# Kernel tuning notes

Measured on AMD Instinct MI355X. Metric: run time of the kernel, lower is better.

The kernel has to match this reference:

```python
import jax, jax.numpy as jnp
import numpy as np

B, S = 32, 128          # batch, seq_len
C, K = 256, 128         # num_concept, dim_k (== dim_e == dim_correct)
DC = 128                # dim_correct
NQ, NIT, NUT = 10000, 1024, 1024


def _xavier(k, shape):
    fan_out, fan_in = shape[0], shape[1]
    bound = float(np.sqrt(6.0 / (fan_in + fan_out)))
    return jax.random.uniform(k, shape, jnp.float32, -bound, bound)


def setup_inputs() -> dict:
    key = jax.random.key(0)
    ks = jax.random.split(key, 16)
    question_seq = jax.random.randint(ks[0], (B, S), 0, NQ + 1)
    interval_time_seq = jax.random.randint(ks[1], (B, S), 0, NIT + 1)
    use_time_seq = jax.random.randint(ks[2], (B, S), 0, NUT + 1)
    correct_seq = jnp.round(jax.random.uniform(ks[3], (B, S))).astype(jnp.float32)
    E_q = _xavier(ks[4], (NQ + 1, K))
    E_it = _xavier(ks[5], (NIT + 1, K))
    E_ut = _xavier(ks[6], (NUT + 1, K))
    q_matrix = (jax.random.uniform(ks[7], (NQ + 1, C)) < 0.03).astype(jnp.float32)
    h0 = _xavier(ks[8], (C, K))  # xavier init of the initial concept memory
    W1 = _xavier(ks[9], (K, K + K + DC)); b1 = jnp.zeros((K,), jnp.float32)
    W2 = _xavier(ks[10], (K, 4 * K));     b2 = jnp.zeros((K,), jnp.float32)
    W3 = _xavier(ks[11], (K, 4 * K));     b3 = jnp.zeros((K,), jnp.float32)
    W4 = _xavier(ks[12], (K, 3 * K));     b4 = jnp.zeros((K,), jnp.float32)
    W5 = _xavier(ks[13], (K, 2 * K));     b5 = jnp.zeros((K,), jnp.float32)
    return dict(question_seq=question_seq, interval_time_seq=interval_time_seq,
                use_time_seq=use_time_seq, correct_seq=correct_seq,
                E_q=E_q, E_it=E_it, E_ut=E_ut, q_matrix=q_matrix, h0=h0,
                W1=W1, b1=b1, W2=W2, b2=b2, W3=W3, b3=b3,
                W4=W4, b4=b4, W5=W5, b5=b5)


def _forward(question_seq, interval_time_seq, use_time_seq, correct_seq,
             E_q, E_it, E_ut, q_matrix, h0,
             W1, b1, W2, b2, W3, b3, W4, b4, W5, b5):
    bsz, slen = question_seq.shape
    dim_k = h0.shape[1]
    dim_c = W1.shape[1] - 2 * dim_k

    q_emb = E_q[question_seq]            # [B,S,K]
    it_emb = E_it[interval_time_seq]     # [B,S,K]
    ut_emb = E_ut[use_time_seq]          # [B,S,K]
    c_emb = jnp.broadcast_to(correct_seq[..., None], (bsz, slen, dim_c))
    all_learning = jnp.concatenate([q_emb, ut_emb, c_emb], -1) @ W1.T + b1  # [B,S,K]
    qe = q_matrix[question_seq]          # [B,S,C]

    h_pre0 = jnp.tile(h0[None], (bsz, 1, 1))                     # [B,C,K]
    h_tilde0 = jnp.einsum('bc,bck->bk', qe[:, 0], h_pre0)        # q_e @ h at t=0
    learning0 = jnp.zeros((bsz, dim_k), all_learning.dtype)

    # split linear_4 weight over its (h_pre, LG, it) concat blocks
    W4h, W4l, W4i = W4[:, :dim_k], W4[:, dim_k:2 * dim_k], W4[:, 2 * dim_k:]

    # time-major per-step inputs for t = 0 .. S-2
    xs = (jnp.swapaxes(it_emb[:, :-1], 0, 1),
          jnp.swapaxes(all_learning[:, :-1], 0, 1),
          jnp.swapaxes(qe[:, :-1], 0, 1),
          jnp.swapaxes(qe[:, 1:], 0, 1),
          jnp.swapaxes(q_emb[:, 1:], 0, 1))

    def step(carry, x):
        h_pre, h_tilde_pre, learning_pre = carry
        it, learning, qe_t, qe_n, qemb_n = x
        cat = jnp.concatenate([learning_pre, it, learning, h_tilde_pre], -1)  # [B,4K]
        learning_gain = jnp.tanh(cat @ W2.T + b2)
        gamma_l = jax.nn.sigmoid(cat @ W3.T + b3)
        LG = gamma_l * (learning_gain + 1.0) * 0.5                 # [B,K]
        LG_tilde = qe_t[:, :, None] * LG[:, None, :]               # [B,C,K] outer write
        gamma_f = jax.nn.sigmoid(jnp.einsum('bck,jk->bcj', h_pre, W4h)
                                 + (LG @ W4l.T + it @ W4i.T + b4)[:, None, :])
        h = LG_tilde + gamma_f * h_pre                             # [B,C,K]
        h_tilde = jnp.einsum('bc,bck->bk', qe_n, h)                # read for t+1
        y = jax.nn.sigmoid(jnp.concatenate([qemb_n, h_tilde], -1) @ W5.T + b5).sum(-1) / dim_k
        return (h, h_tilde, learning), y

    _, ys = jax.lax.scan(step, (h_pre0, h_tilde0, learning0), xs)  # ys: [S-1,B]
    pred = jnp.concatenate([jnp.zeros((bsz, 1), ys.dtype), ys.T], axis=1)
    return pred


def reference(question_seq, interval_time_seq, use_time_seq, correct_seq,
              E_q, E_it, E_ut, q_matrix, h0,
              W1, b1, W2, b2, W3, b3, W4, b4, W5, b5):
    return _forward(question_seq, interval_time_seq, use_time_seq, correct_seq,
                    E_q, E_it, E_ut, q_matrix, h0,
                    W1, b1, W2, b2, W3, b3, W4, b4, W5, b5)
```

## Files before the change

kernel.cpp:

```cpp
#include <hip/hip_runtime.h>
#include <hip/hip_bf16.h>


typedef __bf16 bf16x8 __attribute__((ext_vector_type(8)));
typedef __bf16 bf16x4 __attribute__((ext_vector_type(4)));
typedef float f32x4 __attribute__((ext_vector_type(4)));

#define HBUF 32768

__device__ __forceinline__ float sigmf(float x){
  return __builtin_amdgcn_rcpf(1.0f + __expf(-x));
}

__device__ __forceinline__ bf16x8 cvt8(float4 a, float4 b){
  bf16x8 r;
  r[0]=(__bf16)a.x; r[1]=(__bf16)a.y; r[2]=(__bf16)a.z; r[3]=(__bf16)a.w;
  r[4]=(__bf16)b.x; r[5]=(__bf16)b.y; r[6]=(__bf16)b.z; r[7]=(__bf16)b.w;
  return r;
}

__device__ __forceinline__ void mk_hilo(float4 a, float4 b, bf16x8& hi, bf16x8& lo){
  float v[8] = {a.x,a.y,a.z,a.w,b.x,b.y,b.z,b.w};
  #pragma unroll
  for (int i = 0; i < 8; i++){
    __bf16 h = (__bf16)v[i];
    hi[i] = h;
    lo[i] = (__bf16)(v[i] - (float)h);
  }
}

__device__ __forceinline__ f32x4 mfma16(bf16x8 a, bf16x8 b, f32x4 c){
  return __builtin_amdgcn_mfma_f32_16x16x32_bf16(a, b, c, 0, 0, 0);
}

__device__ __forceinline__ float dpp_sum16(float v){
  int x;
  x = __builtin_amdgcn_update_dpp(0, __builtin_bit_cast(int, v), 0x111, 0xf, 0xf, true);
  v += __builtin_bit_cast(float, x);
  x = __builtin_amdgcn_update_dpp(0, __builtin_bit_cast(int, v), 0x112, 0xf, 0xf, true);
  v += __builtin_bit_cast(float, x);
  x = __builtin_amdgcn_update_dpp(0, __builtin_bit_cast(int, v), 0x114, 0xf, 0xf, true);
  v += __builtin_bit_cast(float, x);
  x = __builtin_amdgcn_update_dpp(0, __builtin_bit_cast(int, v), 0x118, 0xf, 0xf, true);
  v += __builtin_bit_cast(float, x);
  return v;
}

__device__ __forceinline__ void red16(f32x4& r){
  r[0] = dpp_sum16(r[0]);
  r[1] = dpp_sum16(r[1]);
  r[2] = dpp_sum16(r[2]);
  r[3] = dpp_sum16(r[3]);
}

__global__ __launch_bounds__(256) void k1_al(
    const int* __restrict__ qseq, const int* __restrict__ utseq,
    const float* __restrict__ corr,
    const float* __restrict__ Eq, const float* __restrict__ Eut,
    const float* __restrict__ W1, const float* __restrict__ b1,
    const float* __restrict__ W5, const float* __restrict__ b5,
    float* __restrict__ AL, float* __restrict__ pre5)
{
  __shared__ __bf16 inA[64*256];
  __shared__ float corrs[64];
  __shared__ float b1s[128], b5s[128], rsp[256];
  const int tid = threadIdx.x, blk = blockIdx.x;
  if (tid < 128){ b1s[tid]=b1[tid]; b5s[tid]=b5[tid]; }
  {
    int j = tid & 127, hf = tid >> 7;
    const float* p = W1 + j*384 + 256 + hf*64;
    float s = 0.f;
    for (int i = 0; i < 64; i++) s += p[i];
    rsp[tid] = s;
  }
  {
    int r = tid >> 2, seg = tid & 3;
    int R = blk*64 + r;
    int qi = qseq[R], ui = utseq[R];
    if (seg == 0) corrs[r] = corr[R];
    for (int i = 0; i < 64; i++){
      int col = seg*64 + i;
      float v = (col < 128) ? Eq[qi*128 + col] : Eut[ui*128 + (col-128)];
      inA[((r*256 + col) ^ ((r&7)<<3))] = (__bf16)v;
    }
  }
  __syncthreads();
  const int w = tid >> 6, lane = tid & 63;
  const int la = lane & 15, g = lane >> 4;
  const int rbase = w*16;
  bf16x8 af[8];
  #pragma unroll
  for (int kt = 0; kt < 8; kt++){
    int idx = ((rbase+la)*256 + kt*32 + g*8) ^ ((la&7)<<3);
    af[kt] = *(const bf16x8*)&inA[idx];
  }
  for (int jt = 0; jt < 8; jt++){
    f32x4 acc = {0.f,0.f,0.f,0.f};
    const float* Wb = W1 + (jt*16+la)*384;
    #pragma unroll
    for (int kt = 0; kt < 8; kt++){
      const float* p = Wb + kt*32 + g*8;
      acc = mfma16(af[kt], cvt8(*(const float4*)p, *(const float4*)(p+4)), acc);
    }
    int j = jt*16 + la;
    float rsj = rsp[j] + rsp[j+128];
    #pragma unroll
    for (int rr = 0; rr < 4; rr++){
      int row = rbase + g*4 + rr;
      int R = blk*64 + row;
      AL[R*128 + j] = acc[rr] + b1s[j] + corrs[row]*rsj;
    }
  }
  for (int jt = 0; jt < 8; jt++){
    f32x4 acc = {0.f,0.f,0.f,0.f};
    const float* Wb = W5 + (jt*16+la)*256;
    #pragma unroll
    for (int kt = 0; kt < 4; kt++){
      const float* p = Wb + kt*32 + g*8;
      acc = mfma16(af[kt], cvt8(*(const float4*)p, *(const float4*)(p+4)), acc);
    }
    int j = jt*16 + la;
    #pragma unroll
    for (int rr = 0; rr < 4; rr++){
      int row = rbase + g*4 + rr;
      int R = blk*64 + row;
      pre5[R*128 + j] = acc[rr] + b5s[j];
    }
  }
}

__global__ __launch_bounds__(256) void k2_pre(
    const int* __restrict__ itseq, const float* __restrict__ Eit,
    const float* __restrict__ AL,
    const float* __restrict__ W2, const float* __restrict__ W3,
    const float* __restrict__ W4,
    const float* __restrict__ b2, const float* __restrict__ b3,
    const float* __restrict__ b4,
    float* __restrict__ pre23, float* __restrict__ pre4)
{
  __shared__ __bf16 inA[64*384];
  __shared__ int obase[64];
  __shared__ float b2s[128], b3s[128], b4s[128];
  const int tid = threadIdx.x, blk = blockIdx.x;
  if (tid < 128){ b2s[tid]=b2[tid]; b3s[tid]=b3[tid]; b4s[tid]=b4[tid]; }
  {
    int r = tid >> 2, seg = tid & 3;
    int R = blk*64 + r;
    bool valid = (R < 4064);
    int b_ = R / 127, tau = R % 127;
    if (seg == 0) obase[r] = valid ? (b_*127 + tau) : -1;
    int itv = valid ? itseq[b_*128 + tau] : 0;
    for (int i = 0; i < 96; i++){
      int col = seg*96 + i;
      float v = 0.f;
      if (valid){
        if (col < 128)      v = (tau > 0) ? AL[(b_*128 + tau-1)*128 + col] : 0.f;
        else if (col < 256) v = Eit[itv*128 + (col-128)];
        else                v = AL[(b_*128 + tau)*128 + (col-256)];
      }
      inA[((r*384 + col) ^ ((r&7)<<3))] = (__bf16)v;
    }
  }
  __syncthreads();
  const int w = tid >> 6, lane = tid & 63;
  const int la = lane & 15, g = lane >> 4;
  const int rbase = w*16;
  bf16x8 af[12];
  #pragma unroll
  for (int kt = 0; kt < 12; kt++){
    int idx = ((rbase+la)*384 + kt*32 + g*8) ^ ((la&7)<<3);
    af[kt] = *(const bf16x8*)&inA[idx];
  }
  for (int jt = 0; jt < 16; jt++){
    f32x4 acc = {0.f,0.f,0.f,0.f};
    int j = jt*16 + la;
    const float* Wb = (j < 128) ? (W2 + j*512) : (W3 + (j-128)*512);
    #pragma unroll
    for (int kt = 0; kt < 12; kt++){
      const float* p = Wb + kt*32 + g*8;
      acc = mfma16(af[kt], cvt8(*(const float4*)p, *(const float4*)(p+4)), acc);
    }
    float bias = (j < 128) ? b2s[j] : b3s[j-128];
    #pragma unroll
    for (int rr = 0; rr < 4; rr++){
      int row = rbase + g*4 + rr;
      int ob = obase[row];
      if (ob >= 0) pre23[ob*256 + j] = acc[rr] + bias;
    }
  }
  for (int jt = 0; jt < 8; jt++){
    f32x4 acc = {0.f,0.f,0.f,0.f};
    int j = jt*16 + la;
    const float* Wb = W4 + j*384 + 256;
    #pragma unroll
    for (int kk = 0; kk < 4; kk++){
      const float* p = Wb + kk*32 + g*8;
      acc = mfma16(af[4+kk], cvt8(*(const float4*)p, *(const float4*)(p+4)), acc);
    }
    #pragma unroll
    for (int rr = 0; rr < 4; rr++){
      int row = rbase + g*4 + rr;
      int ob = obase[row];
      if (ob >= 0) pre4[ob*128 + j] = acc[rr] + b4s[j];
    }
  }
}

#define SCAN_LDS_BYTES (35136*4)

__global__ __launch_bounds__(512, 2) void lpkt_scan(
    const float* __restrict__ qmat, const int* __restrict__ qseq,
    const float* __restrict__ h0,
    const float* __restrict__ W2, const float* __restrict__ W3,
    const float* __restrict__ W4,
    const float* __restrict__ pre23, const float* __restrict__ pre4,
    float* __restrict__ hist)
{
  extern __shared__ float lds[];
  __bf16* hB   = (__bf16*)lds;
  float*  htb0 = lds + 32768;
  float*  htb1 = lds + 33024;
  float*  LGb  = lds + 33280;
  __bf16* LGh  = (__bf16*)(lds + 33408);
  float*  qeb  = lds + 33472;
  float*  p23L = lds + 34240;
  float*  p4L  = lds + 34752;
  int*    qsl  = (int*)(lds + 35008);

  const int tid  = threadIdx.x;
  const int b    = blockIdx.x;
  const int lane = tid & 63;
  const int w    = tid >> 6;
  const int la   = lane & 15, g = lane >> 4;
  const int jq   = w & 3;
  const int ch   = w >> 2;

  bf16x8 af[2][4];
  bf16x8 af4l[2][4];
  #pragma unroll
  for (int jj = 0; jj < 2; jj++){
    #pragma unroll
    for (int kt = 0; kt < 4; kt++){
      const float* ph = W4 + ((jq*2+jj)*16+la)*384 + kt*32 + g*8;
      const float* pl = W4 + ((jq*2+jj)*16+la)*384 + 128 + kt*32 + g*8;
      af[jj][kt]   = cvt8(*(const float4*)ph, *(const float4*)(ph+4));
      af4l[jj][kt] = cvt8(*(const float4*)pl, *(const float4*)(pl+4));
    }
  }
  bf16x8 af23[2][4];
  #pragma unroll
  for (int kt = 0; kt < 4; kt++){
    const float* p2 = W2 + (w*16+la)*512 + 384 + kt*32 + g*8;
    const float* p3 = W3 + (w*16+la)*512 + 384 + kt*32 + g*8;
    af23[0][kt] = cvt8(*(const float4*)p2, *(const float4*)(p2+4));
    af23[1][kt] = cvt8(*(const float4*)p3, *(const float4*)(p3+4));
  }

  int rb[8], wb[8];
  #pragma unroll
  for (int cg = 0; cg < 8; cg++){
    const int cblk = ch*8 + cg;
    rb[cg] = cblk*2048 + g*128 + la*8;
    wb[cg] = cblk*2048 + jq*512 + (g>>1)*128 + la*8 + (g&1)*4;
  }

  if (tid < 128) qsl[tid] = qseq[b*128 + tid];
  __syncthreads();
  const float* pre23b = pre23 + b*127*256;
  const float* pre4b  = pre4  + b*127*128;
  if (tid < 64)       *(float4*)&qeb[tid*4] = *(const float4*)(qmat + (size_t)qsl[0]*256 + tid*4);
  else if (tid < 128) *(float4*)&qeb[256 + (tid-64)*4] = *(const float4*)(qmat + (size_t)qsl[1]*256 + (tid-64)*4);
  else if (tid < 192) *(float4*)&p23L[(tid-128)*4] = *(const float4*)(pre23b + (tid-128)*4);
  else if (tid < 224) *(float4*)&p4L[(tid-192)*4]  = *(const float4*)(pre4b  + (tid-192)*4);

  float4 hreg[8][2];
  #pragma unroll
  for (int cg = 0; cg < 8; cg++){
    const int c_ = ch*128 + cg*16 + la;
    #pragma unroll
    for (int jj = 0; jj < 2; jj++){
      const int k0 = (jq*2+jj)*16 + g*4;
      float4 v = *(const float4*)(h0 + c_*128 + k0);
      hreg[cg][jj] = v;
      bf16x4 hb; hb[0]=(__bf16)v.x; hb[1]=(__bf16)v.y; hb[2]=(__bf16)v.z; hb[3]=(__bf16)v.w;
      *(bf16x4*)&hB[wb[cg] + jj*256] = hb;
    }
  }
  __syncthreads();
  {
    f32x4 r0 = {0.f,0.f,0.f,0.f}, r1 = {0.f,0.f,0.f,0.f};
    #pragma unroll
    for (int cg = 0; cg < 8; cg++){
      const int c_ = ch*128 + cg*16 + la;
      float q = qeb[c_];
      float4 h0v = hreg[cg][0], h1v = hreg[cg][1];
      r0[0] += q*h0v.x; r0[1] += q*h0v.y; r0[2] += q*h0v.z; r0[3] += q*h0v.w;
      r1[0] += q*h1v.x; r1[1] += q*h1v.y; r1[2] += q*h1v.z; r1[3] += q*h1v.w;
    }
    red16(r0); red16(r1);
    if (la == 15){
      float4 s0 = {r0[0],r0[1],r0[2],r0[3]};
      float4 s1 = {r1[0],r1[1],r1[2],r1[3]};
      *(float4*)&htb0[ch*128 + jq*32 + g*4]      = s0;
      *(float4*)&htb0[ch*128 + jq*32 + 16 + g*4] = s1;
    }
  }
  __syncthreads();

  int i0 = 0, i1 = 1, i2 = 2;

  for (int tau = 0; tau < 127; tau++){
    float* htc = (tau & 1) ? htb1 : htb0;
    float* htn = (tau & 1) ? htb0 : htb1;
    float* qec = qeb + i0*256;
    float* qen = qeb + i1*256;
    float* qep = qeb + i2*256;
    const float* p23c = p23L + (tau & 1)*256;
    const float* p4c  = p4L  + (tau & 1)*128;
    const int roff = (tau & 1) ? HBUF : 0;
    const int woff = (tau & 1) ? 0 : HBUF;

    {
      bf16x8 xh[4], xl[4];
      #pragma unroll
      for (int kt = 0; kt < 4; kt++){
        int k0 = kt*32 + g*8;
        float4 a0 = *(const float4*)&htc[k0];
        float4 a1 = *(const float4*)&htc[k0+4];
        float4 b0 = *(const float4*)&htc[128 + k0];
        float4 b1v = *(const float4*)&htc[128 + k0+4];
        a0.x += b0.x; a0.y += b0.y; a0.z += b0.z; a0.w += b0.w;
        a1.x += b1v.x; a1.y += b1v.y; a1.z += b1v.z; a1.w += b1v.w;
        mk_hilo(a0, a1, xh[kt], xl[kt]);
      }
      f32x4 aLh = {0.f,0.f,0.f,0.f}, aLl = {0.f,0.f,0.f,0.f};
      f32x4 aGh = {0.f,0.f,0.f,0.f}, aGl = {0.f,0.f,0.f,0.f};
      #pragma unroll
      for (int kt = 0; kt < 4; kt++){
        aLh = mfma16(af23[0][kt], xh[kt], aLh);
        aLl = mfma16(af23[0][kt], xl[kt], aLl);
        aGh = mfma16(af23[1][kt], xh[kt], aGh);
        aGl = mfma16(af23[1][kt], xl[kt], aGl);
      }
      float4 lp4 = *(const float4*)&p23c[w*16 + g*4];
      float4 gp4 = *(const float4*)&p23c[128 + w*16 + g*4];
      float4 LG4;
      LG4.x = sigmf(aGh[0]+aGl[0]+gp4.x) * sigmf(2.f*(aLh[0]+aLl[0]+lp4.x));
      LG4.y = sigmf(aGh[1]+aGl[1]+gp4.y) * sigmf(2.f*(aLh[1]+aLl[1]+lp4.y));
      LG4.z = sigmf(aGh[2]+aGl[2]+gp4.z) * sigmf(2.f*(aLh[2]+aLl[2]+lp4.z));
      LG4.w = sigmf(aGh[3]+aGl[3]+gp4.w) * sigmf(2.f*(aLh[3]+aLl[3]+lp4.w));
      if (la == 0){
        *(float4*)&LGb[w*16 + g*4] = LG4;
        bf16x4 lgp;
        lgp[0]=(__bf16)LG4.x; lgp[1]=(__bf16)LG4.y;
        lgp[2]=(__bf16)LG4.z; lgp[3]=(__bf16)LG4.w;
        *(bf16x4*)&LGh[w*16 + g*4] = lgp;
      }
    }
    __syncthreads();

    float4 pf23, pf4, pfqe;
    const bool dopf = (tau < 126);
    const bool do23 = dopf && (tid < 64);
    const bool do4  = dopf && (tid >= 64) && (tid < 96);
    const bool doqe = dopf && (tid >= 448);
    if (do23) pf23 = *(const float4*)(pre23b + (tau+1)*256 + tid*4);
    if (do4)  pf4  = *(const float4*)(pre4b  + (tau+1)*128 + (tid-64)*4);
    if (doqe) pfqe = *(const float4*)(qmat + (size_t)qsl[tau+2]*256 + (tid-448)*4);
    if (tau > 0 && tid >= 96 && tid < 128){
      int i = (tid - 96)*4;
      float4 v0 = *(const float4*)&htc[i];
      float4 v1 = *(const float4*)&htc[128 + i];
      float4 v = {v0.x+v1.x, v0.y+v1.y, v0.z+v1.z, v0.w+v1.w};
      *(float4*)(hist + ((size_t)b*127 + (tau-1))*128 + i) = v;
    }

    float4 z4[2];
    {
      bf16x8 lh[4];
      #pragma unroll
      for (int kt = 0; kt < 4; kt++)
        lh[kt] = *(const bf16x8*)&LGh[kt*32 + g*8];
      #pragma unroll
      for (int jj = 0; jj < 2; jj++){
        f32x4 az = {0.f,0.f,0.f,0.f};
        #pragma unroll
        for (int kt = 0; kt < 4; kt++)
          az = mfma16(af4l[jj][kt], lh[kt], az);
        float4 zp = *(const float4*)&p4c[(jq*2+jj)*16 + g*4];
        z4[jj].x = az[0]+zp.x; z4[jj].y = az[1]+zp.y;
        z4[jj].z = az[2]+zp.z; z4[jj].w = az[3]+zp.w;
      }
    }
    float4 lg4[2];
    #pragma unroll
    for (int jj = 0; jj < 2; jj++)
      lg4[jj] = *(const float4*)&LGb[(jq*2+jj)*16 + g*4];

    bf16x8 bA[4], bB[4];
    {
      const int base = rb[0] + roff;
      #pragma unroll
      for (int kt = 0; kt < 4; kt++) bA[kt] = *(const bf16x8*)&hB[base + kt*512];
    }
    f32x4 r0 = {0.f,0.f,0.f,0.f}, r1 = {0.f,0.f,0.f,0.f};
    #pragma unroll
    for (int cg = 0; cg < 8; cg++){
      const bf16x8* cur = (cg & 1) ? bB : bA;
      bf16x8*       nxt = (cg & 1) ? bA : bB;
      if (cg < 7){
        const int base = rb[cg+1] + roff;
        #pragma unroll
        for (int kt = 0; kt < 4; kt++) nxt[kt] = *(const bf16x8*)&hB[base + kt*512];
      }
      const int c_ = ch*128 + cg*16 + la;
      const float qe_t = qec[c_], qe_n = qen[c_];
      const int wbase = wb[cg] + woff;
      #pragma unroll
      for (int jj = 0; jj < 2; jj++){
        f32x4 acc = {0.f,0.f,0.f,0.f};
        #pragma unroll
        for (int kt = 0; kt < 4; kt++)
          acc = mfma16(af[jj][kt], cur[kt], acc);
        float4 hp = hreg[cg][jj];
        float4 hn;
        hn.x = qe_t*lg4[jj].x + sigmf(acc[0] + z4[jj].x)*hp.x;
        hn.y = qe_t*lg4[jj].y + sigmf(acc[1] + z4[jj].y)*hp.y;
        hn.z = qe_t*lg4[jj].z + sigmf(acc[2] + z4[jj].z)*hp.z;
        hn.w = qe_t*lg4[jj].w + sigmf(acc[3] + z4[jj].w)*hp.w;
        hreg[cg][jj] = hn;
        bf16x4 hb; hb[0]=(__bf16)hn.x; hb[1]=(__bf16)hn.y; hb[2]=(__bf16)hn.z; hb[3]=(__bf16)hn.w;
        *(bf16x4*)&hB[wbase + jj*256] = hb;
        f32x4& r = (jj == 0) ? r0 : r1;
        r[0] += qe_n*hn.x; r[1] += qe_n*hn.y;
        r[2] += qe_n*hn.z; r[3] += qe_n*hn.w;
      }
    }
    red16(r0); red16(r1);
    if (la == 15){
      float4 s0 = {r0[0],r0[1],r0[2],r0[3]};
      float4 s1 = {r1[0],r1[1],r1[2],r1[3]};
      *(float4*)&htn[ch*128 + jq*32 + g*4]      = s0;
      *(float4*)&htn[ch*128 + jq*32 + 16 + g*4] = s1;
    }
    if (do23) *(float4*)&p23L[((tau+1)&1)*256 + tid*4] = pf23;
    if (do4)  *(float4*)&p4L[((tau+1)&1)*128 + (tid-64)*4] = pf4;
    if (doqe) *(float4*)&qep[(tid-448)*4] = pfqe;
    __syncthreads();
    int t_ = i0; i0 = i1; i1 = i2; i2 = t_;
  }

  if (tid < 32){
    int i = tid*4;
    float4 v0 = *(const float4*)&htb1[i];
    float4 v1 = *(const float4*)&htb1[128 + i];
    float4 v = {v0.x+v1.x, v0.y+v1.y, v0.z+v1.z, v0.w+v1.w};
    *(float4*)(hist + ((size_t)b*127 + 126)*128 + i) = v;
  }
}

__global__ __launch_bounds__(128) void k4_y(
    const float* __restrict__ hist, const float* __restrict__ pre5,
    const float* __restrict__ W5, float* __restrict__ out)
{
  const int R = blockIdx.x;
  const int s = R & 127, b = R >> 7;
  const int j = threadIdx.x;
  __shared__ float xs[128];
  __shared__ float partial[2];
  if (s == 0){ if (j == 0) out[R] = 0.f; return; }
  xs[j] = hist[((size_t)b*127 + (s-1))*128 + j];
  __syncthreads();
  const float* wr = W5 + j*256 + 128;
  float acc = pre5[(size_t)R*128 + j];
  #pragma unroll
  for (int k = 0; k < 128; k += 4){
    float4 wv = *(const float4*)&wr[k];
    float4 xv = *(const float4*)&xs[k];
    acc += wv.x*xv.x + wv.y*xv.y + wv.z*xv.z + wv.w*xv.w;
  }
  float v = sigmf(acc);
  #pragma unroll
  for (int m = 1; m < 64; m <<= 1) v += __shfl_xor(v, m);
  if ((j & 63) == 0) partial[j >> 6] = v;
  __syncthreads();
  if (j == 0) out[R] = (partial[0] + partial[1]) * (1.f/128.f);
}

extern "C" void kernel_launch(void* const* d_in, const int* in_sizes, int n_in,
                              void* d_out, int out_size, void* d_ws, size_t ws_size,
                              hipStream_t stream) {
  const int*   qseq  = (const int*)  d_in[0];
  const int*   itseq = (const int*)  d_in[1];
  const int*   utseq = (const int*)  d_in[2];
  const float* corr  = (const float*)d_in[3];
  const float* Eq    = (const float*)d_in[4];
  const float* Eit   = (const float*)d_in[5];
  const float* Eut   = (const float*)d_in[6];
  const float* qmat  = (const float*)d_in[7];
  const float* h0    = (const float*)d_in[8];
  const float* W1    = (const float*)d_in[9];
  const float* b1    = (const float*)d_in[10];
  const float* W2    = (const float*)d_in[11];
  const float* b2    = (const float*)d_in[12];
  const float* W3    = (const float*)d_in[13];
  const float* b3    = (const float*)d_in[14];
  const float* W4    = (const float*)d_in[15];
  const float* b4    = (const float*)d_in[16];
  const float* W5    = (const float*)d_in[17];
  const float* b5    = (const float*)d_in[18];
  float* out = (float*)d_out;

  float* ws    = (float*)d_ws;
  float* AL    = ws;
  float* hist  = ws;
  float* pre5  = ws + 524288;
  float* pre23 = ws + 1048576;
  float* pre4  = ws + 2088960;

  (void)hipFuncSetAttribute(reinterpret_cast<const void*>(&lpkt_scan),
                            hipFuncAttributeMaxDynamicSharedMemorySize,
                            SCAN_LDS_BYTES);

  hipLaunchKernelGGL(k1_al, dim3(64), dim3(256), 0, stream,
                     qseq, utseq, corr, Eq, Eut, W1, b1, W5, b5, AL, pre5);
  hipLaunchKernelGGL(k2_pre, dim3(64), dim3(256), 0, stream,
                     itseq, Eit, AL, W2, W3, W4, b2, b3, b4, pre23, pre4);
  hipLaunchKernelGGL(lpkt_scan, dim3(32), dim3(512), SCAN_LDS_BYTES, stream,
                     qmat, qseq, h0, W2, W3, W4, pre23, pre4, hist);
  hipLaunchKernelGGL(k4_y, dim3(4096), dim3(128), 0, stream,
                     hist, pre5, W5, out);
}
```

Measured before the change: 821.8 us.

## Split each batch's concept memory across two workgroups with global-memory flag exchange

The recurrent scan now launches two workgroups per batch element, each owning half of the 256 concepts and half the LDS state. Every step, each half publishes its partial h_tilde read to a global buffer and sets a release flag, then spin-waits on the peer's flag before summing both partials. This doubles the number of CUs working on the latency-bound serial scan and halves per-block work per step. In exchange it adds a cross-workgroup handshake per timestep through global memory, assumes both peer blocks are co-resident, and carries a bounded spin that could silently continue with stale data.

```diff
diff --git a/kernel.cpp b/kernel.cpp
--- a/kernel.cpp
+++ b/kernel.cpp
@@ -6,7 +6,7 @@
 typedef __bf16 bf16x4 __attribute__((ext_vector_type(4)));
 typedef float f32x4 __attribute__((ext_vector_type(4)));
 
-#define HBUF 32768
+#define HBUF 16384
 
 __device__ __forceinline__ float sigmf(float x){
   return __builtin_amdgcn_rcpf(1.0f + __expf(-x));
@@ -206,7 +206,7 @@
   }
 }
 
-#define SCAN_LDS_BYTES (35136*4)
+#define SCAN_LDS_BYTES (18752*4)
 
 __global__ __launch_bounds__(512, 2) void lpkt_scan(
     const float* __restrict__ qmat, const int* __restrict__ qseq,
@@ -214,27 +214,34 @@
     const float* __restrict__ W2, const float* __restrict__ W3,
     const float* __restrict__ W4,
     const float* __restrict__ pre23, const float* __restrict__ pre4,
-    float* __restrict__ hist)
+    float* __restrict__ hist, float* __restrict__ xbuf, int* __restrict__ flags)
 {
   extern __shared__ float lds[];
   __bf16* hB   = (__bf16*)lds;
-  float*  htb0 = lds + 32768;
-  float*  htb1 = lds + 33024;
-  float*  LGb  = lds + 33280;
-  __bf16* LGh  = (__bf16*)(lds + 33408);
-  float*  qeb  = lds + 33472;
-  float*  p23L = lds + 34240;
-  float*  p4L  = lds + 34752;
-  int*    qsl  = (int*)(lds + 35008);
+  float*  htb0 = lds + 16384;
+  float*  htb1 = lds + 16640;
+  float*  LGb  = lds + 16896;
+  __bf16* LGh  = (__bf16*)(lds + 17024);
+  float*  qeb  = lds + 17088;
+  float*  p23L = lds + 17856;
+  float*  p4L  = lds + 18368;
+  int*    qsl  = (int*)(lds + 18624);
 
   const int tid  = threadIdx.x;
-  const int b    = blockIdx.x;
+  const int bid  = blockIdx.x;
+  const int half = bid >> 5;
+  const int b    = bid & 31;
   const int lane = tid & 63;
   const int w    = tid >> 6;
   const int la   = lane & 15, g = lane >> 4;
   const int jq   = w & 3;
   const int ch   = w >> 2;
 
+  float* xmine = xbuf + ((size_t)(b*2 + half))*128*128;
+  const float* xpeer = xbuf + ((size_t)(b*2 + (half^1)))*128*128;
+  int* fmine = flags + (b*2 + half)*128;
+  const int* fpeer = flags + (b*2 + (half^1))*128;
+
   bf16x8 af[2][4];
   bf16x8 af4l[2][4];
   #pragma unroll
@@ -256,10 +263,10 @@
     af23[1][kt] = cvt8(*(const float4*)p3, *(const float4*)(p3+4));
   }
 
-  int rb[8], wb[8];
-  #pragma unroll
-  for (int cg = 0; cg < 8; cg++){
-    const int cblk = ch*8 + cg;
+  int rb[4], wb[4];
+  #pragma unroll
+  for (int cg = 0; cg < 4; cg++){
+    const int cblk = ch*4 + cg;
     rb[cg] = cblk*2048 + g*128 + la*8;
     wb[cg] = cblk*2048 + jq*512 + (g>>1)*128 + la*8 + (g&1)*4;
   }
@@ -273,10 +280,10 @@
   else if (tid < 192) *(float4*)&p23L[(tid-128)*4] = *(const float4*)(pre23b + (tid-128)*4);
   else if (tid < 224) *(float4*)&p4L[(tid-192)*4]  = *(const float4*)(pre4b  + (tid-192)*4);
 
-  float4 hreg[8][2];
-  #pragma unroll
-  for (int cg = 0; cg < 8; cg++){
-    const int c_ = ch*128 + cg*16 + la;
+  float4 hreg[4][2];
+  #pragma unroll
+  for (int cg = 0; cg < 4; cg++){
+    const int c_ = half*128 + ch*64 + cg*16 + la;
     #pragma unroll
     for (int jj = 0; jj < 2; jj++){
       const int k0 = (jq*2+jj)*16 + g*4;
@@ -290,8 +297,8 @@
   {
     f32x4 r0 = {0.f,0.f,0.f,0.f}, r1 = {0.f,0.f,0.f,0.f};
     #pragma unroll
-    for (int cg = 0; cg < 8; cg++){
-      const int c_ = ch*128 + cg*16 + la;
+    for (int cg = 0; cg < 4; cg++){
+      const int c_ = half*128 + ch*64 + cg*16 + la;
       float q = qeb[c_];
       float4 h0v = hreg[cg][0], h1v = hreg[cg][1];
       r0[0] += q*h0v.x; r0[1] += q*h0v.y; r0[2] += q*h0v.z; r0[3] += q*h0v.w;
@@ -320,6 +327,26 @@
     const int roff = (tau & 1) ? HBUF : 0;
     const int woff = (tau & 1) ? 0 : HBUF;
 
+    if (w == 0){
+      if (lane < 32){
+        float4 v0 = *(const float4*)&htc[lane*4];
+        float4 v1 = *(const float4*)&htc[128 + lane*4];
+        float4 v = {v0.x+v1.x, v0.y+v1.y, v0.z+v1.z, v0.w+v1.w};
+        *(float4*)(xmine + (size_t)tau*128 + lane*4) = v;
+      }
+      __threadfence();
+      if (lane == 0)
+        __hip_atomic_store(&fmine[tau], 1, __ATOMIC_RELEASE, __HIP_MEMORY_SCOPE_AGENT);
+    }
+    {
+      int it = 0;
+      while (__hip_atomic_load(&fpeer[tau], __ATOMIC_ACQUIRE, __HIP_MEMORY_SCOPE_AGENT) == 0){
+        __builtin_amdgcn_s_sleep(2);
+        if (++it > (1 << 22)) break;
+      }
+    }
+    const float* xp = xpeer + (size_t)tau*128;
+
     {
       bf16x8 xh[4], xl[4];
       #pragma unroll
@@ -329,8 +356,12 @@
         float4 a1 = *(const float4*)&htc[k0+4];
         float4 b0 = *(const float4*)&htc[128 + k0];
         float4 b1v = *(const float4*)&htc[128 + k0+4];
-        a0.x += b0.x; a0.y += b0.y; a0.z += b0.z; a0.w += b0.w;
-        a1.x += b1v.x; a1.y += b1v.y; a1.z += b1v.z; a1.w += b1v.w;
+        float4 c0 = *(const float4*)(xp + k0);
+        float4 c1 = *(const float4*)(xp + k0 + 4);
+        a0.x += b0.x + c0.x; a0.y += b0.y + c0.y;
+        a0.z += b0.z + c0.z; a0.w += b0.w + c0.w;
+        a1.x += b1v.x + c1.x; a1.y += b1v.y + c1.y;
+        a1.z += b1v.z + c1.z; a1.w += b1v.w + c1.w;
         mk_hilo(a0, a1, xh[kt], xl[kt]);
       }
       f32x4 aLh = {0.f,0.f,0.f,0.f}, aLl = {0.f,0.f,0.f,0.f};
@@ -367,11 +398,12 @@
     if (do23) pf23 = *(const float4*)(pre23b + (tau+1)*256 + tid*4);
     if (do4)  pf4  = *(const float4*)(pre4b  + (tau+1)*128 + (tid-64)*4);
     if (doqe) pfqe = *(const float4*)(qmat + (size_t)qsl[tau+2]*256 + (tid-448)*4);
-    if (tau > 0 && tid >= 96 && tid < 128){
+    if (half == 0 && tau > 0 && tid >= 96 && tid < 128){
       int i = (tid - 96)*4;
       float4 v0 = *(const float4*)&htc[i];
       float4 v1 = *(const float4*)&htc[128 + i];
-      float4 v = {v0.x+v1.x, v0.y+v1.y, v0.z+v1.z, v0.w+v1.w};
+      float4 v2 = *(const float4*)(xp + i);
+      float4 v = {v0.x+v1.x+v2.x, v0.y+v1.y+v2.y, v0.z+v1.z+v2.z, v0.w+v1.w+v2.w};
       *(float4*)(hist + ((size_t)b*127 + (tau-1))*128 + i) = v;
     }
 
@@ -405,15 +437,15 @@
     }
     f32x4 r0 = {0.f,0.f,0.f,0.f}, r1 = {0.f,0.f,0.f,0.f};
     #pragma unroll
-    for (int cg = 0; cg < 8; cg++){
+    for (int cg = 0; cg < 4; cg++){
       const bf16x8* cur = (cg & 1) ? bB : bA;
       bf16x8*       nxt = (cg & 1) ? bA : bB;
-      if (cg < 7){
+      if (cg < 3){
         const int base = rb[cg+1] + roff;
         #pragma unroll
         for (int kt = 0; kt < 4; kt++) nxt[kt] = *(const bf16x8*)&hB[base + kt*512];
       }
-      const int c_ = ch*128 + cg*16 + la;
+      const int c_ = half*128 + ch*64 + cg*16 + la;
       const float qe_t = qec[c_], qe_n = qen[c_];
       const int wbase = wb[cg] + woff;
       #pragma unroll
@@ -450,12 +482,32 @@
     int t_ = i0; i0 = i1; i1 = i2; i2 = t_;
   }
 
-  if (tid < 32){
-    int i = tid*4;
-    float4 v0 = *(const float4*)&htb1[i];
-    float4 v1 = *(const float4*)&htb1[128 + i];
-    float4 v = {v0.x+v1.x, v0.y+v1.y, v0.z+v1.z, v0.w+v1.w};
-    *(float4*)(hist + ((size_t)b*127 + 126)*128 + i) = v;
+  if (half == 1){
+    if (w == 0){
+      if (lane < 32){
+        float4 v0 = *(const float4*)&htb1[lane*4];
+        float4 v1 = *(const float4*)&htb1[128 + lane*4];
+        float4 v = {v0.x+v1.x, v0.y+v1.y, v0.z+v1.z, v0.w+v1.w};
+        *(float4*)(xmine + (size_t)127*128 + lane*4) = v;
+      }
+      __threadfence();
+      if (lane == 0)
+        __hip_atomic_store(&fmine[127], 1, __ATOMIC_RELEASE, __HIP_MEMORY_SCOPE_AGENT);
+    }
+  } else {
+    if (tid < 32){
+      int it = 0;
+      while (__hip_atomic_load(&fpeer[127], __ATOMIC_ACQUIRE, __HIP_MEMORY_SCOPE_AGENT) == 0){
+        __builtin_amdgcn_s_sleep(2);
+        if (++it > (1 << 22)) break;
+      }
+      int i = tid*4;
+      float4 v0 = *(const float4*)&htb1[i];
+      float4 v1 = *(const float4*)&htb1[128 + i];
+      float4 v2 = *(const float4*)(xpeer + (size_t)127*128 + i);
+      float4 v = {v0.x+v1.x+v2.x, v0.y+v1.y+v2.y, v0.z+v1.z+v2.z, v0.w+v1.w+v2.w};
+      *(float4*)(hist + ((size_t)b*127 + 126)*128 + i) = v;
+    }
   }
 }
 
@@ -517,17 +569,20 @@
   float* pre5  = ws + 524288;
   float* pre23 = ws + 1048576;
   float* pre4  = ws + 2088960;
+  float* xbuf  = ws + 2609152;
+  int*   flags = (int*)(ws + 3657728);
 
   (void)hipFuncSetAttribute(reinterpret_cast<const void*>(&lpkt_scan),
                             hipFuncAttributeMaxDynamicSharedMemorySize,
                             SCAN_LDS_BYTES);
 
+  hipMemsetAsync(flags, 0, 64*128*sizeof(int), stream);
   hipLaunchKernelGGL(k1_al, dim3(64), dim3(256), 0, stream,
                      qseq, utseq, corr, Eq, Eut, W1, b1, W5, b5, AL, pre5);
   hipLaunchKernelGGL(k2_pre, dim3(64), dim3(256), 0, stream,
                      itseq, Eit, AL, W2, W3, W4, b2, b3, b4, pre23, pre4);
-  hipLaunchKernelGGL(lpkt_scan, dim3(32), dim3(512), SCAN_LDS_BYTES, stream,
-                     qmat, qseq, h0, W2, W3, W4, pre23, pre4, hist);
+  hipLaunchKernelGGL(lpkt_scan, dim3(64), dim3(512), SCAN_LDS_BYTES, stream,
+                     qmat, qseq, h0, W2, W3, W4, pre23, pre4, hist, xbuf, flags);
   hipLaunchKernelGGL(k4_y, dim3(4096), dim3(128), 0, stream,
                      hist, pre5, W5, out);
 }
```

Result: slower. 1.842 ms (+124.1%).

## Repartition scan waves, compute forget-gate LG term once, fuse output kernel into scan

Applied to the files above, without the earlier changes.

Each wave now covers 4 output column tiles over 64 concepts instead of 2 tiles over 128 concepts. The per-step LG@W4l term is computed once per wave into shared memory rather than redundantly in every wave, at the cost of an extra barrier per step. The h_tilde partial sums from different waves are combined with LDS atomicAdd into a single buffer, which must be zeroed each step. The separate k4_y output kernel is removed and its work runs at the end of the scan kernel, saving a launch but running on only 32 blocks.

```diff
diff --git a/kernel.cpp b/kernel.cpp
--- a/kernel.cpp
+++ b/kernel.cpp
@@ -6,7 +6,7 @@
 typedef __bf16 bf16x4 __attribute__((ext_vector_type(4)));
 typedef float f32x4 __attribute__((ext_vector_type(4)));
 
-#define HBUF 32768
+#define HBUF 16384*2
 
 __device__ __forceinline__ float sigmf(float x){
   return __builtin_amdgcn_rcpf(1.0f + __expf(-x));
@@ -206,62 +206,64 @@
   }
 }
 
-#define SCAN_LDS_BYTES (35136*4)
+#define SCAN_LDS_BYTES (35008*4)
 
 __global__ __launch_bounds__(512, 2) void lpkt_scan(
     const float* __restrict__ qmat, const int* __restrict__ qseq,
     const float* __restrict__ h0,
     const float* __restrict__ W2, const float* __restrict__ W3,
-    const float* __restrict__ W4,
+    const float* __restrict__ W4, const float* __restrict__ W5,
     const float* __restrict__ pre23, const float* __restrict__ pre4,
-    float* __restrict__ hist)
+    const float* __restrict__ pre5,
+    float* __restrict__ hist, float* __restrict__ out)
 {
   extern __shared__ float lds[];
   __bf16* hB   = (__bf16*)lds;
   float*  htb0 = lds + 32768;
-  float*  htb1 = lds + 33024;
-  float*  LGb  = lds + 33280;
-  __bf16* LGh  = (__bf16*)(lds + 33408);
-  float*  qeb  = lds + 33472;
-  float*  p23L = lds + 34240;
-  float*  p4L  = lds + 34752;
-  int*    qsl  = (int*)(lds + 35008);
+  float*  htb1 = lds + 32896;
+  float*  LGb  = lds + 33024;
+  float*  zb   = lds + 33152;
+  __bf16* LGh  = (__bf16*)(lds + 33280);
+  float*  qeb  = lds + 33344;
+  float*  p23L = lds + 34112;
+  float*  p4L  = lds + 34624;
+  int*    qsl  = (int*)(lds + 34880);
 
   const int tid  = threadIdx.x;
   const int b    = blockIdx.x;
   const int lane = tid & 63;
   const int w    = tid >> 6;
   const int la   = lane & 15, g = lane >> 4;
-  const int jq   = w & 3;
-  const int ch   = w >> 2;
-
-  bf16x8 af[2][4];
-  bf16x8 af4l[2][4];
-  #pragma unroll
-  for (int jj = 0; jj < 2; jj++){
+  const int jh   = w & 1;
+  const int cq   = w >> 1;
+
+  bf16x8 af[4][4];
+  #pragma unroll
+  for (int jj = 0; jj < 4; jj++){
     #pragma unroll
     for (int kt = 0; kt < 4; kt++){
-      const float* ph = W4 + ((jq*2+jj)*16+la)*384 + kt*32 + g*8;
-      const float* pl = W4 + ((jq*2+jj)*16+la)*384 + 128 + kt*32 + g*8;
-      af[jj][kt]   = cvt8(*(const float4*)ph, *(const float4*)(ph+4));
-      af4l[jj][kt] = cvt8(*(const float4*)pl, *(const float4*)(pl+4));
-    }
-  }
+      const float* ph = W4 + ((jh*4+jj)*16+la)*384 + kt*32 + g*8;
+      af[jj][kt] = cvt8(*(const float4*)ph, *(const float4*)(ph+4));
+    }
+  }
+  bf16x8 af4l[4];
   bf16x8 af23[2][4];
   #pragma unroll
   for (int kt = 0; kt < 4; kt++){
+    const float* pl = W4 + (w*16+la)*384 + 128 + kt*32 + g*8;
     const float* p2 = W2 + (w*16+la)*512 + 384 + kt*32 + g*8;
     const float* p3 = W3 + (w*16+la)*512 + 384 + kt*32 + g*8;
+    af4l[kt]    = cvt8(*(const float4*)pl, *(const float4*)(pl+4));
     af23[0][kt] = cvt8(*(const float4*)p2, *(const float4*)(p2+4));
     af23[1][kt] = cvt8(*(const float4*)p3, *(const float4*)(p3+4));
   }
 
-  int rb[8], wb[8];
-  #pragma unroll
-  for (int cg = 0; cg < 8; cg++){
-    const int cblk = ch*8 + cg;
+  int rb[4], wb[4];
+  #pragma unroll
+  for (int cg = 0; cg < 4; cg++){
+    const int cblk = cq*4 + cg;
     rb[cg] = cblk*2048 + g*128 + la*8;
-    wb[cg] = cblk*2048 + jq*512 + (g>>1)*128 + la*8 + (g&1)*4;
+    wb[cg] = cblk*2048 + jh*1024 + (g>>1)*128 + la*8 + (g&1)*4;
   }
 
   if (tid < 128) qsl[tid] = qseq[b*128 + tid];
@@ -272,14 +274,15 @@
   else if (tid < 128) *(float4*)&qeb[256 + (tid-64)*4] = *(const float4*)(qmat + (size_t)qsl[1]*256 + (tid-64)*4);
   else if (tid < 192) *(float4*)&p23L[(tid-128)*4] = *(const float4*)(pre23b + (tid-128)*4);
   else if (tid < 224) *(float4*)&p4L[(tid-192)*4]  = *(const float4*)(pre4b  + (tid-192)*4);
-
-  float4 hreg[8][2];
-  #pragma unroll
-  for (int cg = 0; cg < 8; cg++){
-    const int c_ = ch*128 + cg*16 + la;
-    #pragma unroll
-    for (int jj = 0; jj < 2; jj++){
-      const int k0 = (jq*2+jj)*16 + g*4;
+  else if (tid < 256){ float4 z4i = {0.f,0.f,0.f,0.f}; *(float4*)&htb0[(tid-224)*4] = z4i; }
+
+  float4 hreg[4][4];
+  #pragma unroll
+  for (int cg = 0; cg < 4; cg++){
+    const int c_ = cq*64 + cg*16 + la;
+    #pragma unroll
+    for (int jj = 0; jj < 4; jj++){
+      const int k0 = (jh*4+jj)*16 + g*4;
       float4 v = *(const float4*)(h0 + c_*128 + k0);
       hreg[cg][jj] = v;
       bf16x4 hb; hb[0]=(__bf16)v.x; hb[1]=(__bf16)v.y; hb[2]=(__bf16)v.z; hb[3]=(__bf16)v.w;
@@ -288,21 +291,28 @@
   }
   __syncthreads();
   {
-    f32x4 r0 = {0.f,0.f,0.f,0.f}, r1 = {0.f,0.f,0.f,0.f};
-    #pragma unroll
-    for (int cg = 0; cg < 8; cg++){
-      const int c_ = ch*128 + cg*16 + la;
+    f32x4 r[4] = {{0.f,0.f,0.f,0.f},{0.f,0.f,0.f,0.f},
+                  {0.f,0.f,0.f,0.f},{0.f,0.f,0.f,0.f}};
+    #pragma unroll
+    for (int cg = 0; cg < 4; cg++){
+      const int c_ = cq*64 + cg*16 + la;
       float q = qeb[c_];
-      float4 h0v = hreg[cg][0], h1v = hreg[cg][1];
-      r0[0] += q*h0v.x; r0[1] += q*h0v.y; r0[2] += q*h0v.z; r0[3] += q*h0v.w;
-      r1[0] += q*h1v.x; r1[1] += q*h1v.y; r1[2] += q*h1v.z; r1[3] += q*h1v.w;
-    }
-    red16(r0); red16(r1);
+      #pragma unroll
+      for (int jj = 0; jj < 4; jj++){
+        float4 hv = hreg[cg][jj];
+        r[jj][0] += q*hv.x; r[jj][1] += q*hv.y;
+        r[jj][2] += q*hv.z; r[jj][3] += q*hv.w;
+      }
+    }
+    #pragma unroll
+    for (int jj = 0; jj < 4; jj++) red16(r[jj]);
     if (la == 15){
-      float4 s0 = {r0[0],r0[1],r0[2],r0[3]};
-      float4 s1 = {r1[0],r1[1],r1[2],r1[3]};
-      *(float4*)&htb0[ch*128 + jq*32 + g*4]      = s0;
-      *(float4*)&htb0[ch*128 + jq*32 + 16 + g*4] = s1;
+      #pragma unroll
+      for (int jj = 0; jj < 4; jj++){
+        const int k0 = (jh*4+jj)*16 + g*4;
+        atomicAdd(&htb0[k0+0], r[jj][0]); atomicAdd(&htb0[k0+1], r[jj][1]);
+        atomicAdd(&htb0[k0+2], r[jj][2]); atomicAdd(&htb0[k0+3], r[jj][3]);
+      }
     }
   }
   __syncthreads();
@@ -320,18 +330,13 @@
     const int roff = (tau & 1) ? HBUF : 0;
     const int woff = (tau & 1) ? 0 : HBUF;
 
+    if (tid < 128) htn[tid] = 0.f;
     {
       bf16x8 xh[4], xl[4];
       #pragma unroll
       for (int kt = 0; kt < 4; kt++){
         int k0 = kt*32 + g*8;
-        float4 a0 = *(const float4*)&htc[k0];
-        float4 a1 = *(const float4*)&htc[k0+4];
-        float4 b0 = *(const float4*)&htc[128 + k0];
-        float4 b1v = *(const float4*)&htc[128 + k0+4];
-        a0.x += b0.x; a0.y += b0.y; a0.z += b0.z; a0.w += b0.w;
-        a1.x += b1v.x; a1.y += b1v.y; a1.z += b1v.z; a1.w += b1v.w;
-        mk_hilo(a0, a1, xh[kt], xl[kt]);
+        mk_hilo(*(const float4*)&htc[k0], *(const float4*)&htc[k0+4], xh[kt], xl[kt]);
       }
       f32x4 aLh = {0.f,0.f,0.f,0.f}, aLl = {0.f,0.f,0.f,0.f};
       f32x4 aGh = {0.f,0.f,0.f,0.f}, aGl = {0.f,0.f,0.f,0.f};
@@ -359,6 +364,25 @@
     }
     __syncthreads();
 
+    {
+      bf16x8 lh[4];
+      #pragma unroll
+      for (int kt = 0; kt < 4; kt++)
+        lh[kt] = *(const bf16x8*)&LGh[kt*32 + g*8];
+      f32x4 az0 = {0.f,0.f,0.f,0.f}, az1 = {0.f,0.f,0.f,0.f};
+      az0 = mfma16(af4l[0], lh[0], az0);
+      az1 = mfma16(af4l[1], lh[1], az1);
+      az0 = mfma16(af4l[2], lh[2], az0);
+      az1 = mfma16(af4l[3], lh[3], az1);
+      if (la == 0){
+        float4 zp = *(const float4*)&p4c[w*16 + g*4];
+        float4 zv = {az0[0]+az1[0]+zp.x, az0[1]+az1[1]+zp.y,
+                     az0[2]+az1[2]+zp.z, az0[3]+az1[3]+zp.w};
+        *(float4*)&zb[w*16 + g*4] = zv;
+      }
+    }
+    __syncthreads();
+
     float4 pf23, pf4, pfqe;
     const bool dopf = (tau < 126);
     const bool do23 = dopf && (tid < 64);
@@ -369,33 +393,16 @@
     if (doqe) pfqe = *(const float4*)(qmat + (size_t)qsl[tau+2]*256 + (tid-448)*4);
     if (tau > 0 && tid >= 96 && tid < 128){
       int i = (tid - 96)*4;
-      float4 v0 = *(const float4*)&htc[i];
-      float4 v1 = *(const float4*)&htc[128 + i];
-      float4 v = {v0.x+v1.x, v0.y+v1.y, v0.z+v1.z, v0.w+v1.w};
-      *(float4*)(hist + ((size_t)b*127 + (tau-1))*128 + i) = v;
-    }
-
-    float4 z4[2];
-    {
-      bf16x8 lh[4];
-      #pragma unroll
-      for (int kt = 0; kt < 4; kt++)
-        lh[kt] = *(const bf16x8*)&LGh[kt*32 + g*8];
-      #pragma unroll
-      for (int jj = 0; jj < 2; jj++){
-        f32x4 az = {0.f,0.f,0.f,0.f};
-        #pragma unroll
-        for (int kt = 0; kt < 4; kt++)
-          az = mfma16(af4l[jj][kt], lh[kt], az);
-        float4 zp = *(const float4*)&p4c[(jq*2+jj)*16 + g*4];
-        z4[jj].x = az[0]+zp.x; z4[jj].y = az[1]+zp.y;
-        z4[jj].z = az[2]+zp.z; z4[jj].w = az[3]+zp.w;
-      }
-    }
-    float4 lg4[2];
-    #pragma unroll
-    for (int jj = 0; jj < 2; jj++)
-      lg4[jj] = *(const float4*)&LGb[(jq*2+jj)*16 + g*4];
+      *(float4*)(hist + ((size_t)b*127 + (tau-1))*128 + i) = *(const float4*)&htc[i];
+    }
+
+    float4 z4[4], lg4[4];
+    #pragma unroll
+    for (int jj = 0; jj < 4; jj++){
+      const int k0 = (jh*4+jj)*16 + g*4;
+      z4[jj]  = *(const float4*)&zb[k0];
+      lg4[jj] = *(const float4*)&LGb[k0];
+    }
 
     bf16x8 bA[4], bB[4];
     {
@@ -403,21 +410,22 @@
       #pragma unroll
       for (int kt = 0; kt < 4; kt++) bA[kt] = *(const bf16x8*)&hB[base + kt*512];
     }
-    f32x4 r0 = {0.f,0.f,0.f,0.f}, r1 = {0.f,0.f,0.f,0.f};
-    #pragma unroll
-    for (int cg = 0; cg < 8; cg++){
+    f32x4 r[4] = {{0.f,0.f,0.f,0.f},{0.f,0.f,0.f,0.f},
+                  {0.f,0.f,0.f,0.f},{0.f,0.f,0.f,0.f}};
+    #pragma unroll
+    for (int cg = 0; cg < 4; cg++){
       const bf16x8* cur = (cg & 1) ? bB : bA;
       bf16x8*       nxt = (cg & 1) ? bA : bB;
-      if (cg < 7){
+      if (cg < 3){
         const int base = rb[cg+1] + roff;
         #pragma unroll
         for (int kt = 0; kt < 4; kt++) nxt[kt] = *(const bf16x8*)&hB[base + kt*512];
       }
-      const int c_ = ch*128 + cg*16 + la;
+      const int c_ = cq*64 + cg*16 + la;
       const float qe_t = qec[c_], qe_n = qen[c_];
       const int wbase = wb[cg] + woff;
       #pragma unroll
-      for (int jj = 0; jj < 2; jj++){
+      for (int jj = 0; jj < 4; jj++){
         f32x4 acc = {0.f,0.f,0.f,0.f};
         #pragma unroll
         for (int kt = 0; kt < 4; kt++)
@@ -431,17 +439,19 @@
         hreg[cg][jj] = hn;
         bf16x4 hb; hb[0]=(__bf16)hn.x; hb[1]=(__bf16)hn.y; hb[2]=(__bf16)hn.z; hb[3]=(__bf16)hn.w;
         *(bf16x4*)&hB[wbase + jj*256] = hb;
-        f32x4& r = (jj == 0) ? r0 : r1;
-        r[0] += qe_n*hn.x; r[1] += qe_n*hn.y;
-        r[2] += qe_n*hn.z; r[3] += qe_n*hn.w;
-      }
-    }
-    red16(r0); red16(r1);
+        r[jj][0] += qe_n*hn.x; r[jj][1] += qe_n*hn.y;
+        r[jj][2] += qe_n*hn.z; r[jj][3] += qe_n*hn.w;
+      }
+    }
+    #pragma unroll
+    for (int jj = 0; jj < 4; jj++) red16(r[jj]);
     if (la == 15){
-      float4 s0 = {r0[0],r0[1],r0[2],r0[3]};
-      float4 s1 = {r1[0],r1[1],r1[2],r1[3]};
-      *(float4*)&htn[ch*128 + jq*32 + g*4]      = s0;
-      *(float4*)&htn[ch*128 + jq*32 + 16 + g*4] = s1;
+      #pragma unroll
+      for (int jj = 0; jj < 4; jj++){
+        const int k0 = (jh*4+jj)*16 + g*4;
+        atomicAdd(&htn[k0+0], r[jj][0]); atomicAdd(&htn[k0+1], r[jj][1]);
+        atomicAdd(&htn[k0+2], r[jj][2]); atomicAdd(&htn[k0+3], r[jj][3]);
+      }
     }
     if (do23) *(float4*)&p23L[((tau+1)&1)*256 + tid*4] = pf23;
     if (do4)  *(float4*)&p4L[((tau+1)&1)*128 + (tid-64)*4] = pf4;
@@ -452,39 +462,39 @@
 
   if (tid < 32){
     int i = tid*4;
-    float4 v0 = *(const float4*)&htb1[i];
-    float4 v1 = *(const float4*)&htb1[128 + i];
-    float4 v = {v0.x+v1.x, v0.y+v1.y, v0.z+v1.z, v0.w+v1.w};
-    *(float4*)(hist + ((size_t)b*127 + 126)*128 + i) = v;
-  }
-}
-
-__global__ __launch_bounds__(128) void k4_y(
-    const float* __restrict__ hist, const float* __restrict__ pre5,
-    const float* __restrict__ W5, float* __restrict__ out)
-{
-  const int R = blockIdx.x;
-  const int s = R & 127, b = R >> 7;
-  const int j = threadIdx.x;
-  __shared__ float xs[128];
-  __shared__ float partial[2];
-  if (s == 0){ if (j == 0) out[R] = 0.f; return; }
-  xs[j] = hist[((size_t)b*127 + (s-1))*128 + j];
+    *(float4*)(hist + ((size_t)b*127 + 126)*128 + i) = *(const float4*)&htb1[i];
+  }
   __syncthreads();
-  const float* wr = W5 + j*256 + 128;
-  float acc = pre5[(size_t)R*128 + j];
-  #pragma unroll
-  for (int k = 0; k < 128; k += 4){
-    float4 wv = *(const float4*)&wr[k];
-    float4 xv = *(const float4*)&xs[k];
-    acc += wv.x*xv.x + wv.y*xv.y + wv.z*xv.z + wv.w*xv.w;
-  }
-  float v = sigmf(acc);
-  #pragma unroll
-  for (int m = 1; m < 64; m <<= 1) v += __shfl_xor(v, m);
-  if ((j & 63) == 0) partial[j >> 6] = v;
-  __syncthreads();
-  if (j == 0) out[R] = (partial[0] + partial[1]) * (1.f/128.f);
+  {
+    const int j = tid & 127, so = tid >> 7;
+    float* ypart = lds;
+    const float* wrow = W5 + j*256 + 128;
+    for (int sc = 0; sc < 128; sc += 4){
+      int s = sc + so;
+      float acc = 0.f;
+      if (s > 0){
+        const float* xr = hist + ((size_t)b*127 + (s-1))*128;
+        acc = pre5[(size_t)(b*128 + s)*128 + j];
+        #pragma unroll
+        for (int k = 0; k < 128; k += 4){
+          float4 wv = *(const float4*)&wrow[k];
+          float4 xv = *(const float4*)&xr[k];
+          acc += wv.x*xv.x + wv.y*xv.y + wv.z*xv.z + wv.w*xv.w;
+        }
+        acc = sigmf(acc);
+      }
+      #pragma unroll
+      for (int m = 1; m < 64; m <<= 1) acc += __shfl_xor(acc, m);
+      if (lane == 0) ypart[w] = acc;
+      __syncthreads();
+      if (tid < 4){
+        int s2 = sc + tid;
+        out[b*128 + s2] = (s2 == 0) ? 0.f
+                        : (ypart[tid*2] + ypart[tid*2+1]) * (1.f/128.f);
+      }
+      __syncthreads();
+    }
+  }
 }
 
 extern "C" void kernel_launch(void* const* d_in, const int* in_sizes, int n_in,
@@ -527,7 +537,6 @@
   hipLaunchKernelGGL(k2_pre, dim3(64), dim3(256), 0, stream,
                      itseq, Eit, AL, W2, W3, W4, b2, b3, b4, pre23, pre4);
   hipLaunchKernelGGL(lpkt_scan, dim3(32), dim3(512), SCAN_LDS_BYTES, stream,
-                     qmat, qseq, h0, W2, W3, W4, pre23, pre4, hist);
-  hipLaunchKernelGGL(k4_y, dim3(4096), dim3(128), 0, stream,
-                     hist, pre5, W5, out);
-}
+                     qmat, qseq, h0, W2, W3, W4, W5, pre23, pre4, pre5,
+                     hist, out);
+}
```

After: 1.392 ms. 1.69x slower.
